# Performance work log

Measured on AMD Instinct MI355X. Metric: run time of the kernel, lower is better.

## Reference

```python
import jax, jax.numpy as jnp
import numpy as np

EPS = 1e-5

def rmsnorm(x, w):
    var = jnp.mean(x * x, axis=-1, keepdims=True)
    return x * jax.lax.rsqrt(var + EPS) * w


def setup_inputs() -> dict:
    key = jax.random.key(0)
    B, L, dim = 4, 2048, 1024
    d_inner, d_state, d_conv, dt_rank = 2 * dim, 16, 4, dim // 16
    ks = jax.random.split(key, 8)
    g = lambda k, shape, scale: (jax.random.normal(k, shape, jnp.float32) * scale)
    return {
        "x": g(ks[0], (B, L, dim), 1.0),
        "rms_w": jnp.ones((dim,), jnp.float32),
        "in_proj": g(ks[1], (dim, 2 * d_inner), dim ** -0.5),
        "conv_w": g(ks[2], (d_inner, d_conv), 0.25),
        "conv_b": jnp.zeros((d_inner,), jnp.float32),
        "x_proj": g(ks[3], (d_inner, dt_rank + 2 * d_state), d_inner ** -0.5),
        "dt_w": g(ks[4], (dt_rank, d_inner), dt_rank ** -0.5),
        # inverse-softplus(0.01): softplus(dt_b) ~ 0.01 at init, standard Mamba dt init
        "dt_b": jnp.full((d_inner,), float(np.log(np.expm1(0.01))), jnp.float32),
        # S4D-real init: A_n = -(n+1)
        "A_log": jnp.log(jnp.broadcast_to(jnp.arange(1, d_state + 1, dtype=jnp.float32), (d_inner, d_state))).copy(),
        "D": jnp.ones((d_inner,), jnp.float32),
        "out_proj": g(ks[5], (d_inner, dim), d_inner ** -0.5),
    }


def _mamba_block(x, rms_w, in_proj, conv_w, conv_b, x_proj, dt_w, dt_b, A_log, D, out_proj):
    B, L, dim = x.shape
    d_inner, K = conv_w.shape
    d_state = A_log.shape[1]
    dt_rank = dt_w.shape[0]

    xn = rmsnorm(x, rms_w)
    xz = xn @ in_proj                      # [B,L,2*d_inner]
    xi, z = jnp.split(xz, 2, axis=-1)

    # causal depthwise conv1d over L
    xc = jax.lax.conv_general_dilated(
        xi.transpose(0, 2, 1),             # [B,C,L]
        conv_w[:, None, :],                # [C,1,K]
        window_strides=(1,), padding=[(K - 1, 0)],
        feature_group_count=d_inner,
    ).transpose(0, 2, 1) + conv_b
    xi = jax.nn.silu(xc)                   # [B,L,d_inner]

    dbc = xi @ x_proj                      # [B,L,dt_rank+2*d_state]
    dt, Bm, Cm = jnp.split(dbc, [dt_rank, dt_rank + d_state], axis=-1)
    delta = jax.nn.softplus(dt @ dt_w + dt_b)  # [B,L,d_inner]
    A = -jnp.exp(A_log)                    # [d_inner,d_state]

    def step(h, inputs):
        d_t, x_t, B_t, C_t = inputs        # [B,d_inner],[B,d_inner],[B,d_state],[B,d_state]
        dA = jnp.exp(d_t[..., None] * A)   # [B,d_inner,d_state]
        h = dA * h + (d_t * x_t)[..., None] * B_t[:, None, :]
        y = jnp.einsum('bds,bs->bd', h, C_t)
        return h, y

    h0 = jnp.zeros((B, d_inner, d_state), x.dtype)
    xs = (delta.transpose(1, 0, 2), xi.transpose(1, 0, 2),
          Bm.transpose(1, 0, 2), Cm.transpose(1, 0, 2))
    _, ys = jax.lax.scan(step, h0, xs)     # ys: [L,B,d_inner]

    y = ys.transpose(1, 0, 2) + xi * D     # D skip connection
    y = y * jax.nn.silu(z)                 # output gate
    return x + y @ out_proj                # residual


def reference(x, rms_w, in_proj, conv_w, conv_b, x_proj, dt_w, dt_b, A_log, D, out_proj):
    return _mamba_block(x, rms_w, in_proj, conv_w, conv_b, x_proj, dt_w, dt_b, A_log, D, out_proj)
```

## Files before the change

### kernel.cpp

```cpp
#include <hip/hip_runtime.h>
#include <hip/hip_bf16.h>
#include <math.h>


#define ROWS 8192
#define DIM 1024
#define DINNER 2048
#define DSTATE 16
#define DTRANK 64
#define LSEQ 2048
#define NCHUNK 32
#define LCHUNK 64

#define LOG2E 1.4426950408889634f

typedef unsigned short ushort;
typedef __attribute__((ext_vector_type(8))) short short8;
typedef __attribute__((ext_vector_type(4))) float float4v;

__device__ inline ushort f2bf(float f) {
    __hip_bfloat16 h = __float2bfloat16(f);
    return *reinterpret_cast<ushort*>(&h);
}
__device__ inline float bf2f(ushort u) {
    union { unsigned int i; float f; } w; w.i = ((unsigned int)u) << 16; return w.f;
}

__device__ inline float fexp2(float x) {
#if __has_builtin(__builtin_amdgcn_exp2f)
    return __builtin_amdgcn_exp2f(x);
#else
    return __expf(x * 0.69314718056f);
#endif
}

__device__ inline void dma16(const void* g, void* l) {
    __builtin_amdgcn_global_load_lds(
        (const __attribute__((address_space(1))) unsigned int*)g,
        (__attribute__((address_space(3))) unsigned int*)l, 16, 0, 0);
}

__global__ __launch_bounds__(256)
void prep_kernel(const float* __restrict__ in_proj, ushort* __restrict__ bt1,
                 const float* __restrict__ out_proj, ushort* __restrict__ bt2,
                 const float* __restrict__ x_proj, ushort* __restrict__ bt3,
                 const float* __restrict__ dt_w, ushort* __restrict__ bt4,
                 const float* __restrict__ x, const float* __restrict__ rms_w,
                 ushort* __restrict__ xn, float* __restrict__ dbc) {
    __shared__ float tld[32][33];
    __shared__ float red[4];
    int bid = blockIdx.x, tid = threadIdx.x;
    if (bid < 6464) {
        const float* in; ushort* outT; int R, C, bx, by;
        if (bid < 4096)      { in = in_proj;  outT = bt1; R = 1024; C = 4096; bx = bid & 127; by = bid >> 7; }
        else if (bid < 6144) { int t = bid - 4096; in = out_proj; outT = bt2; R = 2048; C = 1024; bx = t & 31; by = t >> 5; }
        else if (bid < 6336) { int t = bid - 6144; in = x_proj;  outT = bt3; R = 2048; C = 96;  bx = t % 3;  by = t / 3; }
        else                 { int t = bid - 6336; in = dt_w;    outT = bt4; R = 64;   C = 2048; bx = t & 63; by = t >> 6; }
        int tx = tid & 31, ty = tid >> 5;
#pragma unroll
        for (int k = 0; k < 4; ++k)
            tld[ty + k * 8][tx] = in[(long)(by * 32 + ty + k * 8) * C + bx * 32 + tx];
        __syncthreads();
#pragma unroll
        for (int k = 0; k < 4; ++k)
            outT[(long)(bx * 32 + ty + k * 8) * R + by * 32 + tx] = f2bf(tld[tx][ty + k * 8]);
    } else if (bid < 14656) {
        int row = bid - 6464;
        float4 xv = ((const float4*)(x + (long)row * DIM))[tid];
        float ss = xv.x * xv.x + xv.y * xv.y + xv.z * xv.z + xv.w * xv.w;
        for (int off = 32; off > 0; off >>= 1) ss += __shfl_down(ss, off);
        if ((tid & 63) == 0) red[tid >> 6] = ss;
        __syncthreads();
        float scale = rsqrtf((red[0] + red[1] + red[2] + red[3]) / DIM + 1e-5f);
        float4 wv = ((const float4*)rms_w)[tid];
        ushort4 ov;
        ov.x = f2bf(xv.x * scale * wv.x);
        ov.y = f2bf(xv.y * scale * wv.y);
        ov.z = f2bf(xv.z * scale * wv.z);
        ov.w = f2bf(xv.w * scale * wv.w);
        ((ushort4*)xn)[(long)row * 256 + tid] = ov;
    } else {
        int idx = (bid - 14656) * 256 + tid;
        float4 z = {0.f, 0.f, 0.f, 0.f};
        ((float4*)dbc)[idx] = z;
    }
}

template <int EPI>
__global__ __launch_bounds__(256)
void mfma_gemm_dma(const ushort* __restrict__ A, int lda,
                   const ushort* __restrict__ Bt, int ldbt,
                   void* __restrict__ Cv, int ldc, int K,
                   const float* __restrict__ aux) {
    __shared__ __align__(16) ushort As[128][32];
    __shared__ __align__(16) ushort Bs[128][32];
    int tid = threadIdx.x;
    int wave = tid >> 6, lane = tid & 63;
    int wm = wave >> 1, wn = wave & 1;
    int quad = lane >> 4, l16 = lane & 15;
    int row0 = blockIdx.y * 128, col0 = blockIdx.x * 128;

    int r0 = (wave * 2 + 0) * 16 + (lane >> 2);
    int r1 = (wave * 2 + 1) * 16 + (lane >> 2);
    int ks = (lane & 3) * 8;
    const ushort* a0 = A + (long)(row0 + r0) * lda + ks;
    const ushort* a1 = A + (long)(row0 + r1) * lda + ks;
    const ushort* b0 = Bt + (long)(col0 + r0) * ldbt + ks;
    const ushort* b1 = Bt + (long)(col0 + r1) * ldbt + ks;
    ushort* lA0 = &As[(wave * 2 + 0) * 16][0];
    ushort* lA1 = &As[(wave * 2 + 1) * 16][0];
    ushort* lB0 = &Bs[(wave * 2 + 0) * 16][0];
    ushort* lB1 = &Bs[(wave * 2 + 1) * 16][0];

    float4v acc[4][4] = {};

    for (int k0 = 0; k0 < K; k0 += 32) {
        dma16(a0 + k0, lA0);
        dma16(a1 + k0, lA1);
        dma16(b0 + k0, lB0);
        dma16(b1 + k0, lB1);
        __syncthreads();

        short8 afrag[4], bfrag[4];
#pragma unroll
        for (int i = 0; i < 4; ++i)
            afrag[i] = *reinterpret_cast<const short8*>(&As[wm * 64 + i * 16 + l16][quad * 8]);
#pragma unroll
        for (int j = 0; j < 4; ++j)
            bfrag[j] = *reinterpret_cast<const short8*>(&Bs[wn * 64 + j * 16 + l16][quad * 8]);
#pragma unroll
        for (int i = 0; i < 4; ++i)
#pragma unroll
            for (int j = 0; j < 4; ++j)
                acc[i][j] = __builtin_amdgcn_mfma_f32_16x16x32_bf16(
                    afrag[i], bfrag[j], acc[i][j], 0, 0, 0);
        __syncthreads();
    }

#pragma unroll
    for (int i = 0; i < 4; ++i) {
#pragma unroll
        for (int j = 0; j < 4; ++j) {
            int rbase = row0 + wm * 64 + i * 16 + quad * 4;
            int c = col0 + wn * 64 + j * 16 + l16;
#pragma unroll
            for (int r = 0; r < 4; ++r) {
                float v = acc[i][j][r];
                long idx = (long)(rbase + r) * ldc + c;
                if (EPI == 2) ((float*)Cv)[idx] = v + aux[idx];
                else          ((ushort*)Cv)[idx] = f2bf(v);
            }
        }
    }
}

__global__ __launch_bounds__(256)
void xproj_conv_gemm(const ushort* __restrict__ xz,
                     const float* __restrict__ cw, const float* __restrict__ cb,
                     const ushort* __restrict__ bt3,
                     float* __restrict__ dbc) {
    __shared__ __align__(16) ushort As[128][32];
    __shared__ __align__(16) ushort Bs[128][32];
    int tid = threadIdx.x;
    int wave = tid >> 6, lane = tid & 63;
    int wm = wave >> 1, wn = wave & 1;
    int quad = lane >> 4, l16 = lane & 15;
    int row0 = blockIdx.y * 128;
    int ks0 = blockIdx.x * 512;
    int srow = tid >> 2, sseg = tid & 3;

    int r0 = (wave * 2 + 0) * 16 + (lane >> 2);
    int r1 = (wave * 2 + 1) * 16 + (lane >> 2);
    int ksl = (lane & 3) * 8;
    const ushort* b0 = bt3 + (long)r0 * 2048 + ks0 + ksl;
    const ushort* b1 = bt3 + (long)r1 * 2048 + ks0 + ksl;
    ushort* lB0 = &Bs[(wave * 2 + 0) * 16][0];
    ushort* lB1 = &Bs[(wave * 2 + 1) * 16][0];

    float4v acc[4][4] = {};

    for (int k0 = 0; k0 < 512; k0 += 32) {
        dma16(b0 + k0, lB0);
        dma16(b1 + k0, lB1);
#pragma unroll
        for (int it = 0; it < 2; ++it) {
            int r = srow + it * 64;
            long row = row0 + r;
            int l = (int)(row & (LSEQ - 1));
            int cch = ks0 + k0 + sseg * 8;
            short8 v[4];
#pragma unroll
            for (int t = 0; t < 4; ++t) {
                if (l - 3 + t >= 0) v[t] = *(const short8*)&xz[(row - 3 + t) * 4096 + cch];
                else { short8 zz = {0,0,0,0,0,0,0,0}; v[t] = zz; }
            }
            ushort o[8];
#pragma unroll
            for (int j = 0; j < 8; ++j) {
                float4 w = ((const float4*)cw)[cch + j];
                float a = cb[cch + j]
                        + bf2f((ushort)v[0][j]) * w.x + bf2f((ushort)v[1][j]) * w.y
                        + bf2f((ushort)v[2][j]) * w.z + bf2f((ushort)v[3][j]) * w.w;
                a = a / (1.f + __expf(-a));
                o[j] = f2bf(a);
            }
            *(short8*)&As[r][sseg * 8] = *(const short8*)o;
        }
        __syncthreads();

        short8 afrag[4], bfrag[4];
#pragma unroll
        for (int i = 0; i < 4; ++i)
            afrag[i] = *reinterpret_cast<const short8*>(&As[wm * 64 + i * 16 + l16][quad * 8]);
#pragma unroll
        for (int j = 0; j < 4; ++j)
            bfrag[j] = *reinterpret_cast<const short8*>(&Bs[wn * 64 + j * 16 + l16][quad * 8]);
#pragma unroll
        for (int i = 0; i < 4; ++i)
#pragma unroll
            for (int j = 0; j < 4; ++j)
                acc[i][j] = __builtin_amdgcn_mfma_f32_16x16x32_bf16(
                    afrag[i], bfrag[j], acc[i][j], 0, 0, 0);
        __syncthreads();
    }
#pragma unroll
    for (int i = 0; i < 4; ++i) {
#pragma unroll
        for (int j = 0; j < 4; ++j) {
            int rbase = row0 + wm * 64 + i * 16 + quad * 4;
            int c = wn * 64 + j * 16 + l16;
            if (c < 96) {
#pragma unroll
                for (int r = 0; r < 4; ++r)
                    atomicAdd(&dbc[(long)(rbase + r) * 96 + c], acc[i][j][r]);
            }
        }
    }
}

__global__ __launch_bounds__(256)
void mfma_gemm_dt(const float* __restrict__ A, int lda,
                  const ushort* __restrict__ Bt, int ldbt,
                  ushort* __restrict__ C, int ldc, int K,
                  const float* __restrict__ aux) {
    __shared__ __align__(16) ushort As[128][40];
    __shared__ __align__(16) ushort Bs[128][40];
    int tid = threadIdx.x;
    int wave = tid >> 6, lane = tid & 63;
    int wm = wave >> 1, wn = wave & 1;
    int quad = lane >> 4, l16 = lane & 15;
    int row0 = blockIdx.y * 128, col0 = blockIdx.x * 128;
    int srow = tid >> 2, sseg = tid & 3;

    float4v acc[4][4] = {};

    for (int k0 = 0; k0 < K; k0 += 32) {
#pragma unroll
        for (int it = 0; it < 2; ++it) {
            int r = srow + it * 64;
            const float* ap = A + (long)(row0 + r) * lda + k0 + sseg * 8;
            ushort tmp[8];
#pragma unroll
            for (int j = 0; j < 8; ++j) tmp[j] = f2bf(ap[j]);
            *reinterpret_cast<short8*>(&As[r][sseg * 8]) =
                *reinterpret_cast<const short8*>(tmp);
            const ushort* bp = Bt + (long)(col0 + r) * ldbt + k0 + sseg * 8;
            *reinterpret_cast<short8*>(&Bs[r][sseg * 8]) =
                *reinterpret_cast<const short8*>(bp);
        }
        __syncthreads();
        short8 afrag[4], bfrag[4];
#pragma unroll
        for (int i = 0; i < 4; ++i)
            afrag[i] = *reinterpret_cast<const short8*>(&As[wm * 64 + i * 16 + l16][quad * 8]);
#pragma unroll
        for (int j = 0; j < 4; ++j)
            bfrag[j] = *reinterpret_cast<const short8*>(&Bs[wn * 64 + j * 16 + l16][quad * 8]);
#pragma unroll
        for (int i = 0; i < 4; ++i)
#pragma unroll
            for (int j = 0; j < 4; ++j)
                acc[i][j] = __builtin_amdgcn_mfma_f32_16x16x32_bf16(
                    afrag[i], bfrag[j], acc[i][j], 0, 0, 0);
        __syncthreads();
    }
#pragma unroll
    for (int i = 0; i < 4; ++i) {
#pragma unroll
        for (int j = 0; j < 4; ++j) {
            int rbase = row0 + wm * 64 + i * 16 + quad * 4;
            int c = col0 + wn * 64 + j * 16 + l16;
#pragma unroll
            for (int r = 0; r < 4; ++r) {
                float v = acc[i][j][r] + aux[c];
                v = (v > 20.f) ? v : __logf(1.f + __expf(v));
                C[(long)(rbase + r) * ldc + c] = f2bf(v);
            }
        }
    }
}

__global__ __launch_bounds__(256)
void scan_part1(const ushort* __restrict__ xz,
                const ushort* __restrict__ dlt,
                const float* __restrict__ dbc,
                const float* __restrict__ A_log,
                const float* __restrict__ cw, const float* __restrict__ cb,
                float* __restrict__ hbuf,
                float* __restrict__ sdbuf) {
    int c = blockIdx.y * 256 + threadIdx.x;
    int b = blockIdx.z, g = blockIdx.x;
    float A2[16];
#pragma unroll
    for (int s = 0; s < 16; ++s) A2[s] = -__expf(A_log[c * 16 + s]) * LOG2E;
    float4 w = ((const float4*)cw)[c];
    float cbc = cb[c];
    float h[16] = {};
    float sumd = 0.f;
    long row0 = (long)b * LSEQ + (long)g * LCHUNK;
    int l0 = g * LCHUNK;
    float x0 = (l0 >= 3) ? bf2f(xz[(row0 - 3) * 4096 + c]) : 0.f;
    float x1 = (l0 >= 2) ? bf2f(xz[(row0 - 2) * 4096 + c]) : 0.f;
    float x2 = (l0 >= 1) ? bf2f(xz[(row0 - 1) * 4096 + c]) : 0.f;
    long row = row0;
    for (int l = 0; l < LCHUNK; ++l, ++row) {
        float x3 = bf2f(xz[row * 4096 + c]);
        float xc = cbc + x0 * w.x + x1 * w.y + x2 * w.z + x3 * w.w;
        xc = xc / (1.f + __expf(-xc));
        x0 = x1; x1 = x2; x2 = x3;
        float d = bf2f(dlt[row * 2048 + c]);
        const float* __restrict__ bc = dbc + row * 96;
        sumd += d;
        float dx = d * xc;
#pragma unroll
        for (int s = 0; s < 16; ++s)
            h[s] = fexp2(d * A2[s]) * h[s] + dx * bc[64 + s];
    }
    long hb = ((long)(b * NCHUNK + g) * 16) * 2048 + c;
#pragma unroll
    for (int s = 0; s < 16; ++s) hbuf[hb + (long)s * 2048] = h[s];
    sdbuf[(long)(b * NCHUNK + g) * 2048 + c] = sumd;
}

__global__ __launch_bounds__(256)
void scan_part2(float* __restrict__ hbuf, const float* __restrict__ sdbuf,
                const float* __restrict__ A_log) {
    int gl = blockIdx.x * 256 + threadIdx.x;
    int c = gl & 2047, s = (gl >> 11) & 15, b = gl >> 15;
    float A2 = -__expf(A_log[c * 16 + s]) * LOG2E;
    float hrun = 0.f;
    for (int g = 0; g < NCHUNK; ++g) {
        long hi = ((long)(b * NCHUNK + g) * 16 + s) * 2048 + c;
        float hout = hbuf[hi];
        float sd = sdbuf[(long)(b * NCHUNK + g) * 2048 + c];
        hbuf[hi] = hrun;
        hrun = fexp2(A2 * sd) * hrun + hout;
    }
}

__global__ __launch_bounds__(256)
void scan_part3(const ushort* __restrict__ xz,
                ushort* __restrict__ dlt,
                const float* __restrict__ dbc,
                const float* __restrict__ A_log,
                const float* __restrict__ cw, const float* __restrict__ cb,
                const float* __restrict__ Dp,
                const float* __restrict__ hbuf) {
    int c = blockIdx.y * 256 + threadIdx.x;
    int b = blockIdx.z, g = blockIdx.x;
    float A2[16], h[16];
#pragma unroll
    for (int s = 0; s < 16; ++s) A2[s] = -__expf(A_log[c * 16 + s]) * LOG2E;
    long hb = ((long)(b * NCHUNK + g) * 16) * 2048 + c;
#pragma unroll
    for (int s = 0; s < 16; ++s) h[s] = hbuf[hb + (long)s * 2048];
    float4 w = ((const float4*)cw)[c];
    float cbc = cb[c];
    float Dc = Dp[c];
    long row0 = (long)b * LSEQ + (long)g * LCHUNK;
    int l0 = g * LCHUNK;
    float x0 = (l0 >= 3) ? bf2f(xz[(row0 - 3) * 4096 + c]) : 0.f;
    float x1 = (l0 >= 2) ? bf2f(xz[(row0 - 2) * 4096 + c]) : 0.f;
    float x2 = (l0 >= 1) ? bf2f(xz[(row0 - 1) * 4096 + c]) : 0.f;
    long row = row0;
    for (int l = 0; l < LCHUNK; ++l, ++row) {
        float x3 = bf2f(xz[row * 4096 + c]);
        float xc = cbc + x0 * w.x + x1 * w.y + x2 * w.z + x3 * w.w;
        xc = xc / (1.f + __expf(-xc));
        x0 = x1; x1 = x2; x2 = x3;
        float d = bf2f(dlt[row * 2048 + c]);
        float z = bf2f(xz[row * 4096 + 2048 + c]);
        const float* __restrict__ bc = dbc + row * 96;
        float dx = d * xc;
        float y = 0.f;
#pragma unroll
        for (int s = 0; s < 16; ++s) {
            h[s] = fexp2(d * A2[s]) * h[s] + dx * bc[64 + s];
            y += h[s] * bc[80 + s];
        }
        float yv = (y + xc * Dc) * (z / (1.f + __expf(-z)));
        dlt[row * 2048 + c] = f2bf(yv);
    }
}

extern "C" void kernel_launch(void* const* d_in, const int* in_sizes, int n_in,
                              void* d_out, int out_size, void* d_ws, size_t ws_size,
                              hipStream_t stream) {
    const float* x        = (const float*)d_in[0];
    const float* rms_w    = (const float*)d_in[1];
    const float* in_proj  = (const float*)d_in[2];
    const float* conv_w   = (const float*)d_in[3];
    const float* conv_b   = (const float*)d_in[4];
    const float* x_proj   = (const float*)d_in[5];
    const float* dt_w     = (const float*)d_in[6];
    const float* dt_b     = (const float*)d_in[7];
    const float* A_log    = (const float*)d_in[8];
    const float* Dp       = (const float*)d_in[9];
    const float* out_proj = (const float*)d_in[10];
    float* out = (float*)d_out;

    char* p = (char*)d_ws;
    ushort* xz  = (ushort*)p;   p += (size_t)ROWS * 4096 * 2;
    ushort* dlt = (ushort*)p;   p += (size_t)ROWS * 2048 * 2;
    float*  dbc = (float*)p;    p += (size_t)ROWS * 96 * 4;
    ushort* bt1 = (ushort*)p;   p += (size_t)4096 * 1024 * 2;
    ushort* bt2 = (ushort*)p;   p += (size_t)1024 * 2048 * 2;
    ushort* bt3 = (ushort*)p;   p += (size_t)128 * 2048 * 2;
    ushort* bt4 = (ushort*)p;   p += (size_t)2048 * 64 * 2;
    ushort* xn  = (ushort*)p;   p += (size_t)ROWS * 1024 * 2;
    float* sdbuf = (float*)p;   p += (size_t)4 * NCHUNK * 2048 * 4;
    float* hbuf  = (float*)xn;

    prep_kernel<<<15424, 256, 0, stream>>>(in_proj, bt1, out_proj, bt2,
                                           x_proj, bt3, dt_w, bt4,
                                           x, rms_w, xn, dbc);
    mfma_gemm_dma<0><<<dim3(4096 / 128, ROWS / 128), 256, 0, stream>>>(
        xn, DIM, bt1, 1024, xz, 4096, DIM, nullptr);
    xproj_conv_gemm<<<dim3(4, ROWS / 128), 256, 0, stream>>>(
        xz, conv_w, conv_b, bt3, dbc);
    mfma_gemm_dt<<<dim3(2048 / 128, ROWS / 128), 256, 0, stream>>>(
        dbc, 96, bt4, 64, dlt, 2048, DTRANK, dt_b);
    scan_part1<<<dim3(NCHUNK, DINNER / 256, 4), 256, 0, stream>>>(
        xz, dlt, dbc, A_log, conv_w, conv_b, hbuf, sdbuf);
    scan_part2<<<512, 256, 0, stream>>>(hbuf, sdbuf, A_log);
    scan_part3<<<dim3(NCHUNK, DINNER / 256, 4), 256, 0, stream>>>(
        xz, dlt, dbc, A_log, conv_w, conv_b, Dp, hbuf);
    mfma_gemm_dma<2><<<dim3(DIM / 128, ROWS / 128), 256, 0, stream>>>(
        dlt, 2048, bt2, DINNER, out, DIM, DINNER, x);
}
```

Before: 485.0 us.

## Replace GEMM with 4-stage LDS ring-buffer pipelined kernel and larger tiles

Replaces the single-buffered MFMA GEMM with a templated kernel that keeps a 4-deep LDS ring of K-tiles. It prefetches three tiles ahead using async global-to-LDS DMA, with explicit vmcnt waits and a single barrier per iteration. The LDS layout becomes fragment-major so MFMA operands are read contiguously, and MFMA priority is raised during compute. The in_proj GEMM moves to 256x256 tiles with 8 waves, while out_proj keeps 128x128. This is meant to hide global-load latency and cut barrier stalls, at the cost of much more LDS per block and therefore lower occupancy.

```diff
diff --git a/kernel.cpp b/kernel.cpp
--- a/kernel.cpp
+++ b/kernel.cpp
@@ -86,67 +86,87 @@
     }
 }
 
-template <int EPI>
-__global__ __launch_bounds__(256)
-void mfma_gemm_dma(const ushort* __restrict__ A, int lda,
-                   const ushort* __restrict__ Bt, int ldbt,
-                   void* __restrict__ Cv, int ldc, int K,
-                   const float* __restrict__ aux) {
-    __shared__ __align__(16) ushort As[128][32];
-    __shared__ __align__(16) ushort Bs[128][32];
-    int tid = threadIdx.x;
-    int wave = tid >> 6, lane = tid & 63;
-    int wm = wave >> 1, wn = wave & 1;
-    int quad = lane >> 4, l16 = lane & 15;
-    int row0 = blockIdx.y * 128, col0 = blockIdx.x * 128;
-
-    int r0 = (wave * 2 + 0) * 16 + (lane >> 2);
-    int r1 = (wave * 2 + 1) * 16 + (lane >> 2);
-    int ks = (lane & 3) * 8;
-    const ushort* a0 = A + (long)(row0 + r0) * lda + ks;
-    const ushort* a1 = A + (long)(row0 + r1) * lda + ks;
-    const ushort* b0 = Bt + (long)(col0 + r0) * ldbt + ks;
-    const ushort* b1 = Bt + (long)(col0 + r1) * ldbt + ks;
-    ushort* lA0 = &As[(wave * 2 + 0) * 16][0];
-    ushort* lA1 = &As[(wave * 2 + 1) * 16][0];
-    ushort* lB0 = &Bs[(wave * 2 + 0) * 16][0];
-    ushort* lB1 = &Bs[(wave * 2 + 1) * 16][0];
-
-    float4v acc[4][4] = {};
-
-    for (int k0 = 0; k0 < K; k0 += 32) {
-        dma16(a0 + k0, lA0);
-        dma16(a1 + k0, lA1);
-        dma16(b0 + k0, lB0);
-        dma16(b1 + k0, lB1);
-        __syncthreads();
-
-        short8 afrag[4], bfrag[4];
-#pragma unroll
-        for (int i = 0; i < 4; ++i)
-            afrag[i] = *reinterpret_cast<const short8*>(&As[wm * 64 + i * 16 + l16][quad * 8]);
-#pragma unroll
-        for (int j = 0; j < 4; ++j)
-            bfrag[j] = *reinterpret_cast<const short8*>(&Bs[wn * 64 + j * 16 + l16][quad * 8]);
-#pragma unroll
-        for (int i = 0; i < 4; ++i)
-#pragma unroll
-            for (int j = 0; j < 4; ++j)
-                acc[i][j] = __builtin_amdgcn_mfma_f32_16x16x32_bf16(
-                    afrag[i], bfrag[j], acc[i][j], 0, 0, 0);
-        __syncthreads();
-    }
-
-#pragma unroll
-    for (int i = 0; i < 4; ++i) {
-#pragma unroll
-        for (int j = 0; j < 4; ++j) {
-            int rbase = row0 + wm * 64 + i * 16 + quad * 4;
-            int c = col0 + wn * 64 + j * 16 + l16;
+template <int MW, int NW, int MF, int NF, int EPI>
+__global__ __launch_bounds__(MW * NW * 64, 2)
+void gemm_ring(const ushort* __restrict__ A, int lda,
+               const ushort* __restrict__ Bt, int ldbt,
+               void* __restrict__ Cv, int ldc, int K,
+               const float* __restrict__ aux) {
+    constexpr int W    = MW * NW;
+    constexpr int BLKM = MW * MF * 16;
+    constexpr int BLKN = NW * NF * 16;
+    constexpr int TILE = (BLKM + BLKN) * 32;
+    __shared__ __align__(16) ushort lds[4 * TILE];
+
+    const int tid  = threadIdx.x;
+    const int w    = tid >> 6, lane = tid & 63;
+    const int wm   = w / NW,   wn   = w % NW;
+    const int quad = lane >> 4, l16 = lane & 15;
+    const long row0 = (long)blockIdx.y * BLKM;
+    const long col0 = (long)blockIdx.x * BLKN;
+
+    const ushort* gA0 = A  + (row0 + (w    ) * 16 + l16) * lda  + quad * 8;
+    const ushort* gA1 = A  + (row0 + (w + W) * 16 + l16) * lda  + quad * 8;
+    const ushort* gB0 = Bt + (col0 + (w    ) * 16 + l16) * ldbt + quad * 8;
+    const ushort* gB1 = Bt + (col0 + (w + W) * 16 + l16) * ldbt + quad * 8;
+
+    const int NT = K >> 5;
+    float4v acc[MF][NF] = {};
+
+#define STAGE(kt) do {                                            \
+        ushort* lb_ = lds + ((kt) & 3) * TILE;                    \
+        const int ko_ = (kt) << 5;                                \
+        dma16(gA0 + ko_, lb_ + (w    ) * 512);                    \
+        dma16(gA1 + ko_, lb_ + (w + W) * 512);                    \
+        dma16(gB0 + ko_, lb_ + BLKM * 32 + (w    ) * 512);        \
+        dma16(gB1 + ko_, lb_ + BLKM * 32 + (w + W) * 512);        \
+    } while (0)
+
+    STAGE(0); STAGE(1); STAGE(2);
+    asm volatile("s_waitcnt vmcnt(8)" ::: "memory");
+    __builtin_amdgcn_s_barrier();
+    __builtin_amdgcn_sched_barrier(0);
+
+    for (int t = 0; t < NT; ++t) {
+        const ushort* lb = lds + (t & 3) * TILE;
+        short8 af[MF], bf[NF];
+#pragma unroll
+        for (int m = 0; m < MF; ++m)
+            af[m] = *reinterpret_cast<const short8*>(
+                &lb[(wm * MF + m) * 512 + lane * 8]);
+#pragma unroll
+        for (int n = 0; n < NF; ++n)
+            bf[n] = *reinterpret_cast<const short8*>(
+                &lb[BLKM * 32 + (wn * NF + n) * 512 + lane * 8]);
+        if (t + 3 < NT) STAGE(t + 3);
+        __builtin_amdgcn_s_setprio(1);
+#pragma unroll
+        for (int m = 0; m < MF; ++m)
+#pragma unroll
+            for (int n = 0; n < NF; ++n)
+                acc[m][n] = __builtin_amdgcn_mfma_f32_16x16x32_bf16(
+                    af[m], bf[n], acc[m][n], 0, 0, 0);
+        __builtin_amdgcn_s_setprio(0);
+        if (t < NT - 3)       asm volatile("s_waitcnt vmcnt(8)" ::: "memory");
+        else if (t == NT - 3) asm volatile("s_waitcnt vmcnt(4)" ::: "memory");
+        else if (t == NT - 2) asm volatile("s_waitcnt vmcnt(0)" ::: "memory");
+        if (t < NT - 1) {
+            __builtin_amdgcn_s_barrier();
+            __builtin_amdgcn_sched_barrier(0);
+        }
+    }
+#undef STAGE
+
+#pragma unroll
+    for (int m = 0; m < MF; ++m) {
+#pragma unroll
+        for (int n = 0; n < NF; ++n) {
+            long rbase = row0 + wm * (MF * 16) + m * 16 + quad * 4;
+            long c = col0 + wn * (NF * 16) + n * 16 + l16;
 #pragma unroll
             for (int r = 0; r < 4; ++r) {
-                float v = acc[i][j][r];
-                long idx = (long)(rbase + r) * ldc + c;
+                float v = acc[m][n][r];
+                long idx = (rbase + r) * (long)ldc + c;
                 if (EPI == 2) ((float*)Cv)[idx] = v + aux[idx];
                 else          ((ushort*)Cv)[idx] = f2bf(v);
             }
@@ -434,7 +454,7 @@
     prep_kernel<<<15424, 256, 0, stream>>>(in_proj, bt1, out_proj, bt2,
                                            x_proj, bt3, dt_w, bt4,
                                            x, rms_w, xn, dbc);
-    mfma_gemm_dma<0><<<dim3(4096 / 128, ROWS / 128), 256, 0, stream>>>(
+    gemm_ring<2, 4, 8, 4, 0><<<dim3(4096 / 256, ROWS / 256), 512, 0, stream>>>(
         xn, DIM, bt1, 1024, xz, 4096, DIM, nullptr);
     xproj_conv_gemm<<<dim3(4, ROWS / 128), 256, 0, stream>>>(
         xz, conv_w, conv_b, bt3, dbc);
@@ -445,6 +465,6 @@
     scan_part2<<<512, 256, 0, stream>>>(hbuf, sdbuf, A_log);
     scan_part3<<<dim3(NCHUNK, DINNER / 256, 4), 256, 0, stream>>>(
         xz, dlt, dbc, A_log, conv_w, conv_b, Dp, hbuf);
-    mfma_gemm_dma<2><<<dim3(DIM / 128, ROWS / 128), 256, 0, stream>>>(
-        dlt, 2048, bt2, DINNER, out, DIM, DINNER, x);
-}
+    gemm_ring<2, 2, 4, 4, 2><<<dim3(DIM / 128, ROWS / 128), 256, 0, stream>>>(
+        dlt, DINNER, bt2, DINNER, out, DIM, DINNER, x);
+}
```

Measured after the change: 481.9 us. Within noise of the previous version (-0.6%).
